# Kernel optimization log

Measured on AMD Instinct MI355X. Metric: run time of the kernel, lower is better.

## Reference

```python
import jax, jax.numpy as jnp
import numpy as np
import math

B, S, D, H, R = 4, 2048, 512, 8, 8  # R = k+1 relative slots per direction


def setup_inputs() -> dict:
    key = jax.random.key(0)
    ks = jax.random.split(key, 16)
    dk = D // H
    sc = 1.0 / math.sqrt(D)
    return {
        "query": jax.random.normal(ks[0], (B, S, D), jnp.float32),
        "key": jax.random.normal(ks[1], (B, S, D), jnp.float32),
        "value": jax.random.normal(ks[2], (B, S, D), jnp.float32),
        "start_nodes": jax.random.randint(ks[3], (B, H, R, S), 0, S, jnp.int64 if jax.config.jax_enable_x64 else jnp.int32),
        "end_nodes": jax.random.randint(ks[4], (B, H, R, S), 0, S, jnp.int64 if jax.config.jax_enable_x64 else jnp.int32),
        "rel_q": jax.random.normal(ks[5], (1, H, 2 * R, dk), jnp.float32),
        "rel_k": jax.random.normal(ks[6], (1, H, 2 * R, dk), jnp.float32),
        "rel_v": jax.random.normal(ks[7], (1, H, 2 * R, dk), jnp.float32),
        "Wq": jax.random.normal(ks[8], (D, D), jnp.float32) * sc,
        "bq": jnp.zeros((D,), jnp.float32),
        "Wk": jax.random.normal(ks[9], (D, D), jnp.float32) * sc,
        "bk": jnp.zeros((D,), jnp.float32),
        "Wv": jax.random.normal(ks[10], (D, D), jnp.float32) * sc,
        "bv": jnp.zeros((D,), jnp.float32),
        "Wo": jax.random.normal(ks[11], (D, D), jnp.float32) * sc,
        "bo": jnp.zeros((D,), jnp.float32),
    }


def reference(query, key, value, start_nodes, end_nodes, rel_q, rel_k, rel_v,
              Wq, bq, Wk, bk, Wv, bv, Wo, bo):
    Bs, Ss, Ds = query.shape
    Hs = start_nodes.shape[1]
    dk = Ds // Hs

    def proj(x, W, b):
        return (x @ W.T + b).reshape(Bs, Ss, Hs, dk).transpose(0, 2, 1, 3)  # [B,H,S,dk]

    q = proj(query, Wq, bq)
    k = proj(key, Wk, bk)
    v = proj(value, Wv, bv)

    start_mask = start_nodes == -1
    sn = jnp.where(start_mask, 0, start_nodes)  # -1 padding -> 0 (masked out below)
    qidx = jnp.concatenate([end_nodes, sn], axis=2)  # [B,H,2R,S]
    kidx = jnp.concatenate([sn, end_nodes], axis=2)

    bi = jnp.arange(Bs)[:, None, None, None]
    hi = jnp.arange(Hs)[None, :, None, None]
    q_ctx = q[bi, hi, qidx]  # [B,H,2R,S,dk]
    k_ctx = k[bi, hi, kidx]
    v_ctx = v[bi, hi, kidx]

    # c2c + c2p + p2c, scale_factor = 3 (rel_q and rel_k both provided)
    scores = ((q_ctx * k_ctx).sum(-1)
              + (q_ctx * rel_k[:, :, :, None, :]).sum(-1)
              + (rel_q[:, :, :, None, :] * k_ctx).sum(-1))
    scores = scores / (3.0 * jnp.sqrt(jnp.asarray(dk, scores.dtype)))

    # mask: padded edges masked in both halves; first S flat entries always masked
    mask = jnp.concatenate([start_mask, start_mask], axis=2).reshape(Bs, Hs, -1)
    mask = mask.at[:, :, :Ss].set(True)
    sflat = jnp.exp(jnp.where(mask, -1e9, scores.reshape(Bs, Hs, -1)))  # [B,H,2R*S]

    qf = qidx.reshape(Bs, Hs, -1)
    b2 = jnp.arange(Bs)[:, None, None]
    h2 = jnp.arange(Hs)[None, :, None]
    # scatter-add softmax denominator over destination nodes, then gather back
    denom = jnp.zeros((Bs, Hs, Ss), sflat.dtype).at[b2, h2, qf].add(sflat)
    denom = jnp.where(denom == 0, -1e9, denom)
    probs = (sflat / denom[b2, h2, qf]).reshape(Bs, Hs, -1, Ss, 1)  # [B,H,2R,S,1]

    attn_v = probs * (v_ctx + rel_v[:, :, :, None, :])  # [B,H,2R,S,dk]
    out = jnp.zeros((Bs, Hs, Ss, dk), attn_v.dtype).at[b2, h2, qf].add(
        attn_v.reshape(Bs, Hs, -1, dk))  # scatter-add aggregation over edges

    out = out.transpose(0, 2, 1, 3).reshape(Bs, Ss, Ds)
    return out @ Wo.T + bo
```

## Files before the change

### kernel.cpp

```cpp
#include <hip/hip_runtime.h>
#include <math.h>

#define B_ 4
#define S_ 2048
#define D_ 512
#define H_ 8
#define R_ 8
#define DK_ 64
#define EPB   (2*R_*S_)
#define ELLCAP 64

typedef __attribute__((ext_vector_type(8))) short bf16x8;
typedef __attribute__((ext_vector_type(8))) unsigned short ushort8_t;
typedef __attribute__((ext_vector_type(4))) float f32x4;

#define AS1q const __attribute__((address_space(1)))
#define AS3q __attribute__((address_space(3)))

__device__ inline unsigned short f2bf(float f) {
    unsigned u = __builtin_bit_cast(unsigned, f);
    u += 0x7fffu + ((u >> 16) & 1u);
    return (unsigned short)(u >> 16);
}

__global__ __launch_bounds__(256) void prep_w(
    const float* __restrict__ Wq, const float* __restrict__ Wk,
    const float* __restrict__ Wv, const float* __restrict__ Wo,
    unsigned short* __restrict__ wqb, unsigned short* __restrict__ wkb,
    unsigned short* __restrict__ wvb, unsigned short* __restrict__ wob)
{
    int bid = blockIdx.x;
    int z = bid >> 8;
    const float* x = (z == 0) ? Wq : (z == 1) ? Wk : (z == 2) ? Wv : Wo;
    unsigned short* y = (z == 0) ? wqb : (z == 1) ? wkb : (z == 2) ? wvb : wob;
    size_t i = ((size_t)(bid & 255) * 256 + threadIdx.x) * 4;
    float4 v = *(const float4*)&x[i];
    *(ushort4*)&y[i] = make_ushort4(f2bf(v.x), f2bf(v.y), f2bf(v.z), f2bf(v.w));
}

__global__ __launch_bounds__(256) void gemm_qkv(
    const float* __restrict__ A0, const float* __restrict__ A1,
    const float* __restrict__ A2,
    const unsigned short* __restrict__ W0, const unsigned short* __restrict__ W1,
    const unsigned short* __restrict__ W2,
    const float* __restrict__ bi0, const float* __restrict__ bi1, const float* __restrict__ bi2,
    float* __restrict__ C0, float* __restrict__ C1, float* __restrict__ C2)
{
    __shared__ unsigned short As[128 * 64];
    __shared__ unsigned short Bs[128 * 64];
    const int bi  = blockIdx.x;
    const int xcd = bi & 7;
    const int r   = bi >> 3;
    const int z   = r >> 5;
    const int rr  = r & 31;
    const int m0  = (xcd * 8 + (rr >> 2)) * 128;
    const int n0  = (rr & 3) * 128;

    const float* A          = (z == 0) ? A0 : (z == 1) ? A1 : A2;
    const unsigned short* W = (z == 0) ? W0 : (z == 1) ? W1 : W2;
    const float* bias       = (z == 0) ? bi0 : (z == 1) ? bi1 : bi2;
    float* C                = (z == 0) ? C0 : (z == 1) ? C1 : C2;

    const int t    = threadIdx.x;
    const int lane = t & 63;
    const int w    = t >> 6;
    const int wm   = w >> 1, wn = w & 1;
    const int lr    = lane >> 3;
    const int cglob = (lane & 7) ^ lr;

    f32x4 acc[4][4] = {};

    for (int kk = 0; kk < D_; kk += 64) {
        #pragma unroll
        for (int i = 0; i < 4; ++i) {
            int rowl = w * 32 + i * 8;
            const float* ga = A + (size_t)(m0 + rowl + lr) * D_ + kk + cglob * 8;
            float4 a0 = *(const float4*)ga;
            float4 a1 = *(const float4*)(ga + 4);
            ushort8_t c;
            c[0] = f2bf(a0.x); c[1] = f2bf(a0.y); c[2] = f2bf(a0.z); c[3] = f2bf(a0.w);
            c[4] = f2bf(a1.x); c[5] = f2bf(a1.y); c[6] = f2bf(a1.z); c[7] = f2bf(a1.w);
            *(ushort8_t*)&As[(rowl + lr) * 64 + (lane & 7) * 8] = c;
            const unsigned short* gb =
                W + (size_t)(n0 + rowl + lr) * D_ + kk + cglob * 8;
            __builtin_amdgcn_global_load_lds((AS1q unsigned*)gb,
                (AS3q unsigned*)(Bs + rowl * 64), 16, 0, 0);
        }
        __syncthreads();

        #pragma unroll
        for (int ks = 0; ks < 64; ks += 32) {
            const int c0 = ks >> 3;
            bf16x8 af[4], bfr[4];
            #pragma unroll
            for (int mi = 0; mi < 4; ++mi) {
                int row = wm * 64 + mi * 16 + (lane & 15);
                int cp  = (c0 + (lane >> 4)) ^ (lane & 7);
                af[mi] = *(const bf16x8*)&As[row * 64 + cp * 8];
            }
            #pragma unroll
            for (int nj = 0; nj < 4; ++nj) {
                int row = wn * 64 + nj * 16 + (lane & 15);
                int cp  = (c0 + (lane >> 4)) ^ (lane & 7);
                bfr[nj] = *(const bf16x8*)&Bs[row * 64 + cp * 8];
            }
            #pragma unroll
            for (int mi = 0; mi < 4; ++mi)
                #pragma unroll
                for (int nj = 0; nj < 4; ++nj)
                    acc[mi][nj] = __builtin_amdgcn_mfma_f32_16x16x32_bf16(af[mi], bfr[nj], acc[mi][nj], 0, 0, 0);
        }
        __syncthreads();
    }

    #pragma unroll
    for (int mi = 0; mi < 4; ++mi) {
        #pragma unroll
        for (int nj = 0; nj < 4; ++nj) {
            #pragma unroll
            for (int rg = 0; rg < 4; ++rg) {
                int m = m0 + wm * 64 + mi * 16 + (lane >> 4) * 4 + rg;
                int n = n0 + wn * 64 + nj * 16 + (lane & 15);
                float val = acc[mi][nj][rg] + bias[n];
                int b = m >> 11, s = m & (S_ - 1);
                int h = n >> 6,  d = n & 63;
                C[((((size_t)b * H_ + h) * S_ + s) << 6) + d] = val;
            }
        }
    }
}

__global__ __launch_bounds__(256) void gemm_out(
    const unsigned short* __restrict__ A, const unsigned short* __restrict__ W,
    const float* __restrict__ bias, float* __restrict__ Cf)
{
    __shared__ unsigned short As[128 * 64];
    __shared__ unsigned short Bs[64 * 64];
    const int bi  = blockIdx.x;
    const int xcd = bi & 7;
    const int r   = bi >> 3;
    const int m0  = (xcd * 8 + (r >> 3)) * 128;
    const int n0  = (r & 7) * 64;

    const int t    = threadIdx.x;
    const int lane = t & 63;
    const int w    = t >> 6;
    const int wm   = w >> 1, wn = w & 1;
    const int lr    = lane >> 3;
    const int cglob = (lane & 7) ^ lr;

    f32x4 acc[4][2] = {};

    for (int kk = 0; kk < D_; kk += 64) {
        #pragma unroll
        for (int i = 0; i < 4; ++i) {
            int rowl = w * 32 + i * 8;
            int m = m0 + rowl + lr;
            int b = m >> 11, s = m & (S_ - 1), h = kk >> 6;
            const unsigned short* ga =
                A + ((((size_t)b * H_ + h) * S_ + s) << 6) + cglob * 8;
            __builtin_amdgcn_global_load_lds((AS1q unsigned*)ga,
                (AS3q unsigned*)(As + rowl * 64), 16, 0, 0);
        }
        #pragma unroll
        for (int i = 0; i < 2; ++i) {
            int rowl = w * 16 + i * 8;
            const unsigned short* gb =
                W + (size_t)(n0 + rowl + lr) * D_ + kk + cglob * 8;
            __builtin_amdgcn_global_load_lds((AS1q unsigned*)gb,
                (AS3q unsigned*)(Bs + rowl * 64), 16, 0, 0);
        }
        __syncthreads();

        #pragma unroll
        for (int ks = 0; ks < 64; ks += 32) {
            const int c0 = ks >> 3;
            bf16x8 af[4], bfr[2];
            #pragma unroll
            for (int mi = 0; mi < 4; ++mi) {
                int row = wm * 64 + mi * 16 + (lane & 15);
                int cp  = (c0 + (lane >> 4)) ^ (lane & 7);
                af[mi] = *(const bf16x8*)&As[row * 64 + cp * 8];
            }
            #pragma unroll
            for (int nj = 0; nj < 2; ++nj) {
                int row = wn * 32 + nj * 16 + (lane & 15);
                int cp  = (c0 + (lane >> 4)) ^ (lane & 7);
                bfr[nj] = *(const bf16x8*)&Bs[row * 64 + cp * 8];
            }
            #pragma unroll
            for (int mi = 0; mi < 4; ++mi)
                #pragma unroll
                for (int nj = 0; nj < 2; ++nj)
                    acc[mi][nj] = __builtin_amdgcn_mfma_f32_16x16x32_bf16(af[mi], bfr[nj], acc[mi][nj], 0, 0, 0);
        }
        __syncthreads();
    }

    #pragma unroll
    for (int mi = 0; mi < 4; ++mi) {
        #pragma unroll
        for (int nj = 0; nj < 2; ++nj) {
            #pragma unroll
            for (int rg = 0; rg < 4; ++rg) {
                int m = m0 + wm * 64 + mi * 16 + (lane >> 4) * 4 + rg;
                int n = n0 + wn * 32 + nj * 16 + (lane & 15);
                Cf[(size_t)m * D_ + n] = acc[mi][nj][rg] + bias[n];
            }
        }
    }
}

__global__ __launch_bounds__(1024) void attn_fused(
    const float* __restrict__ q, const float* __restrict__ k_,
    const float* __restrict__ v_,
    const float* __restrict__ rel_q, const float* __restrict__ rel_k,
    const float* __restrict__ rel_v,
    const int* __restrict__ start_nodes, const int* __restrict__ end_nodes,
    unsigned short* __restrict__ attn)
{
    __shared__ unsigned short ell[128 * ELLCAP];
    __shared__ int cnt[128];
    const int bi  = blockIdx.x;
    const int xcd = bi & 7;
    const int loc = bi >> 3;
    const int bh  = xcd * 4 + (loc >> 4);
    const int dlo = (loc & 15) << 7;
    const int t   = threadIdx.x;

    if (t < 128) cnt[t] = 0;
    __syncthreads();

    const int base_idx = bh * (R_ * S_);
    for (int f = t; f < EPB; f += 1024) {
        int r2 = f >> 11;
        if (r2 == 0) continue;
        int s = f & (S_ - 1);
        int idx = base_idx + (r2 & 7) * S_ + s;
        int sn = start_nodes[idx];
        if (sn == -1) continue;
        int en = end_nodes[idx];
        int dst = (r2 < R_) ? en : sn;
        unsigned rel = (unsigned)(dst - dlo);
        if (rel < 128u) {
            int ki = (r2 < R_) ? sn : en;
            int pos = atomicAdd(&cnt[rel], 1);
            if (pos < ELLCAP)
                ell[(rel << 6) + pos] = (unsigned short)((r2 << 11) | ki);
        }
    }
    __syncthreads();

    const int w    = t >> 6;
    const int lane = t & 63;
    const int grp  = lane >> 3;
    const int sub  = lane & 7;
    const int h    = bh & 7;
    const size_t node_base = ((size_t)bh << 11);

    for (int dd = 0; dd < 8; ++dd) {
        int dl  = dd * 16 + w;
        int dst = dlo + dl;

        float qv[8];
        *(float4*)&qv[0] = *(const float4*)&q[((node_base + dst) << 6) + sub * 8];
        *(float4*)&qv[4] = *(const float4*)&q[((node_base + dst) << 6) + sub * 8 + 4];

        int n = cnt[dl];
        if (n > ELLCAP) n = ELLCAP;
        int d_all = (int)ell[(dl << 6) + lane];

        float den = 0.f;
        float o[8] = {};
        #pragma unroll 2
        for (int j = 0; j < n; j += 8) {
            int slot = j + grp;
            int d = __shfl(d_all, slot);
            bool valid = slot < n;
            int ki = d & (S_ - 1);
            int r2 = (d >> 11) & 15;
            size_t koff = ((node_base + ki) << 6) + sub * 8;
            int roff = (((h << 4) + r2) << 6) + sub * 8;
            float kv[8], rqv[8], rkv[8], vv[8], rvv[8];
            *(float4*)&kv[0]  = *(const float4*)&k_[koff];
            *(float4*)&kv[4]  = *(const float4*)&k_[koff + 4];
            *(float4*)&rqv[0] = *(const float4*)&rel_q[roff];
            *(float4*)&rqv[4] = *(const float4*)&rel_q[roff + 4];
            *(float4*)&rkv[0] = *(const float4*)&rel_k[roff];
            *(float4*)&rkv[4] = *(const float4*)&rel_k[roff + 4];
            float p = 0.f;
            #pragma unroll
            for (int i = 0; i < 8; ++i)
                p = fmaf(kv[i], qv[i] + rqv[i], fmaf(qv[i], rkv[i], p));
            p += __shfl_xor(p, 1);
            p += __shfl_xor(p, 2);
            p += __shfl_xor(p, 4);
            float sf = valid ? __expf(p * (1.0f / 24.0f)) : 0.f;
            *(float4*)&vv[0]  = *(const float4*)&v_[koff];
            *(float4*)&vv[4]  = *(const float4*)&v_[koff + 4];
            *(float4*)&rvv[0] = *(const float4*)&rel_v[roff];
            *(float4*)&rvv[4] = *(const float4*)&rel_v[roff + 4];
            den += sf;
            #pragma unroll
            for (int i = 0; i < 8; ++i)
                o[i] = fmaf(sf, vv[i] + rvv[i], o[i]);
        }
        den += __shfl_xor(den, 8); den += __shfl_xor(den, 16); den += __shfl_xor(den, 32);
        #pragma unroll
        for (int i = 0; i < 8; ++i) {
            o[i] += __shfl_xor(o[i], 8);
            o[i] += __shfl_xor(o[i], 16);
            o[i] += __shfl_xor(o[i], 32);
        }
        if (grp == 0) {
            float inv = (den > 0.f) ? 1.0f / den : 0.f;
            ushort8_t rs;
            #pragma unroll
            for (int i = 0; i < 8; ++i) rs[i] = f2bf(o[i] * inv);
            *(ushort8_t*)&attn[((node_base + dst) << 6) + sub * 8] = rs;
        }
    }
}

extern "C" void kernel_launch(void* const* d_in, const int* in_sizes, int n_in,
                              void* d_out, int out_size, void* d_ws, size_t ws_size,
                              hipStream_t stream) {
    const float* query = (const float*)d_in[0];
    const float* key   = (const float*)d_in[1];
    const float* value = (const float*)d_in[2];
    const int* start_nodes = (const int*)d_in[3];
    const int* end_nodes   = (const int*)d_in[4];
    const float* rel_q = (const float*)d_in[5];
    const float* rel_k = (const float*)d_in[6];
    const float* rel_v = (const float*)d_in[7];
    const float* Wq = (const float*)d_in[8];
    const float* bq = (const float*)d_in[9];
    const float* Wk = (const float*)d_in[10];
    const float* bk = (const float*)d_in[11];
    const float* Wv = (const float*)d_in[12];
    const float* bv = (const float*)d_in[13];
    const float* Wo = (const float*)d_in[14];
    const float* bo = (const float*)d_in[15];
    float* out = (float*)d_out;

    const size_t NQ = (size_t)B_ * H_ * S_ * DK_;
    const size_t NW = (size_t)D_ * D_;
    float* qf = (float*)d_ws;
    float* kf = qf + NQ;
    float* vf = kf + NQ;
    unsigned short* attn = (unsigned short*)(vf + NQ);
    unsigned short* wqb  = attn + NQ;
    unsigned short* wkb  = wqb + NW;
    unsigned short* wvb  = wkb + NW;
    unsigned short* wob  = wvb + NW;

    prep_w<<<1024, 256, 0, stream>>>(Wq, Wk, Wv, Wo, wqb, wkb, wvb, wob);

    gemm_qkv<<<768, 256, 0, stream>>>(query, key, value, wqb, wkb, wvb,
                                      bq, bk, bv, qf, kf, vf);

    attn_fused<<<512, 1024, 0, stream>>>(qf, kf, vf, rel_q, rel_k, rel_v,
                                         start_nodes, end_nodes, attn);

    gemm_out<<<512, 256, 0, stream>>>(attn, wob, bo, out);
}
```

Baseline: 237.0 us.

## Store Q/K/V and rel tables in bf16 and pre-pack weights into MFMA fragment layout

```diff
diff --git a/kernel.cpp b/kernel.cpp
--- a/kernel.cpp
+++ b/kernel.cpp
@@ -22,32 +22,71 @@
     u += 0x7fffu + ((u >> 16) & 1u);
     return (unsigned short)(u >> 16);
 }
-
-__global__ __launch_bounds__(256) void prep_w(
+__device__ inline float bf2f(unsigned short u) {
+    return __builtin_bit_cast(float, ((unsigned)u) << 16);
+}
+
+__global__ __launch_bounds__(256) void prep(
+    const float* __restrict__ query, const float* __restrict__ key,
+    const float* __restrict__ value,
     const float* __restrict__ Wq, const float* __restrict__ Wk,
     const float* __restrict__ Wv, const float* __restrict__ Wo,
-    unsigned short* __restrict__ wqb, unsigned short* __restrict__ wkb,
-    unsigned short* __restrict__ wvb, unsigned short* __restrict__ wob)
+    const float* __restrict__ rel_q, const float* __restrict__ rel_k,
+    const float* __restrict__ rel_v,
+    unsigned short* __restrict__ qc, unsigned short* __restrict__ kc_,
+    unsigned short* __restrict__ vc,
+    unsigned short* __restrict__ wqp, unsigned short* __restrict__ wkp,
+    unsigned short* __restrict__ wvp, unsigned short* __restrict__ wop,
+    unsigned short* __restrict__ rqb, unsigned short* __restrict__ rkb,
+    unsigned short* __restrict__ rvb)
 {
     int bid = blockIdx.x;
-    int z = bid >> 8;
-    const float* x = (z == 0) ? Wq : (z == 1) ? Wk : (z == 2) ? Wv : Wo;
-    unsigned short* y = (z == 0) ? wqb : (z == 1) ? wkb : (z == 2) ? wvb : wob;
-    size_t i = ((size_t)(bid & 255) * 256 + threadIdx.x) * 4;
-    float4 v = *(const float4*)&x[i];
-    *(ushort4*)&y[i] = make_ushort4(f2bf(v.x), f2bf(v.y), f2bf(v.z), f2bf(v.w));
+    int t = threadIdx.x;
+    if (bid < 12288) {
+        int z = bid >> 12;
+        const float* x = (z == 0) ? query : (z == 1) ? key : value;
+        unsigned short* y = (z == 0) ? qc : (z == 1) ? kc_ : vc;
+        size_t i = ((size_t)(bid & 4095) * 256 + t) * 4;
+        float4 v = *(const float4*)&x[i];
+        *(ushort4*)&y[i] = make_ushort4(f2bf(v.x), f2bf(v.y), f2bf(v.z), f2bf(v.w));
+    } else if (bid < 12800) {
+        int r = bid - 12288;
+        int z = r >> 7;
+        const float* x = (z == 0) ? Wq : (z == 1) ? Wk : (z == 2) ? Wv : Wo;
+        unsigned short* y = (z == 0) ? wqp : (z == 1) ? wkp : (z == 2) ? wvp : wop;
+        int fi = (r & 127) * 256 + t;
+        int ng   = fi >> 10;
+        int kc   = (fi >> 6) & 15;
+        int lane = fi & 63;
+        const float* src = x + (size_t)(ng * 16 + (lane & 15)) * D_
+                             + kc * 32 + (lane >> 4) * 8;
+        float4 a0 = *(const float4*)src;
+        float4 a1 = *(const float4*)(src + 4);
+        ushort8_t c;
+        c[0] = f2bf(a0.x); c[1] = f2bf(a0.y); c[2] = f2bf(a0.z); c[3] = f2bf(a0.w);
+        c[4] = f2bf(a1.x); c[5] = f2bf(a1.y); c[6] = f2bf(a1.z); c[7] = f2bf(a1.w);
+        *(ushort8_t*)&y[(size_t)fi * 8] = c;
+    } else {
+        int rr = bid - 12800;
+        int z = rr >> 3;
+        const float* x = (z == 0) ? rel_q : (z == 1) ? rel_k : rel_v;
+        unsigned short* y = (z == 0) ? rqb : (z == 1) ? rkb : rvb;
+        size_t i = ((size_t)(rr & 7) * 256 + t) * 4;
+        float4 v = *(const float4*)&x[i];
+        *(ushort4*)&y[i] = make_ushort4(f2bf(v.x), f2bf(v.y), f2bf(v.z), f2bf(v.w));
+    }
 }
 
 __global__ __launch_bounds__(256) void gemm_qkv(
-    const float* __restrict__ A0, const float* __restrict__ A1,
-    const float* __restrict__ A2,
+    const unsigned short* __restrict__ A0, const unsigned short* __restrict__ A1,
+    const unsigned short* __restrict__ A2,
     const unsigned short* __restrict__ W0, const unsigned short* __restrict__ W1,
     const unsigned short* __restrict__ W2,
     const float* __restrict__ bi0, const float* __restrict__ bi1, const float* __restrict__ bi2,
-    float* __restrict__ C0, float* __restrict__ C1, float* __restrict__ C2)
+    unsigned short* __restrict__ C0, unsigned short* __restrict__ C1,
+    unsigned short* __restrict__ C2)
 {
     __shared__ unsigned short As[128 * 64];
-    __shared__ unsigned short Bs[128 * 64];
     const int bi  = blockIdx.x;
     const int xcd = bi & 7;
     const int r   = bi >> 3;
@@ -56,10 +95,10 @@
     const int m0  = (xcd * 8 + (rr >> 2)) * 128;
     const int n0  = (rr & 3) * 128;
 
-    const float* A          = (z == 0) ? A0 : (z == 1) ? A1 : A2;
+    const unsigned short* A = (z == 0) ? A0 : (z == 1) ? A1 : A2;
     const unsigned short* W = (z == 0) ? W0 : (z == 1) ? W1 : W2;
     const float* bias       = (z == 0) ? bi0 : (z == 1) ? bi1 : bi2;
-    float* C                = (z == 0) ? C0 : (z == 1) ? C1 : C2;
+    unsigned short* C       = (z == 0) ? C0 : (z == 1) ? C1 : C2;
 
     const int t    = threadIdx.x;
     const int lane = t & 63;
@@ -74,23 +113,17 @@
         #pragma unroll
         for (int i = 0; i < 4; ++i) {
             int rowl = w * 32 + i * 8;
-            const float* ga = A + (size_t)(m0 + rowl + lr) * D_ + kk + cglob * 8;
-            float4 a0 = *(const float4*)ga;
-            float4 a1 = *(const float4*)(ga + 4);
-            ushort8_t c;
-            c[0] = f2bf(a0.x); c[1] = f2bf(a0.y); c[2] = f2bf(a0.z); c[3] = f2bf(a0.w);
-            c[4] = f2bf(a1.x); c[5] = f2bf(a1.y); c[6] = f2bf(a1.z); c[7] = f2bf(a1.w);
-            *(ushort8_t*)&As[(rowl + lr) * 64 + (lane & 7) * 8] = c;
-            const unsigned short* gb =
-                W + (size_t)(n0 + rowl + lr) * D_ + kk + cglob * 8;
-            __builtin_amdgcn_global_load_lds((AS1q unsigned*)gb,
-                (AS3q unsigned*)(Bs + rowl * 64), 16, 0, 0);
+            const unsigned short* ga =
+                A + (size_t)(m0 + rowl + lr) * D_ + kk + cglob * 8;
+            __builtin_amdgcn_global_load_lds((AS1q unsigned*)ga,
+                (AS3q unsigned*)(As + rowl * 64), 16, 0, 0);
         }
         __syncthreads();
 
         #pragma unroll
         for (int ks = 0; ks < 64; ks += 32) {
             const int c0 = ks >> 3;
+            const int kc = (kk + ks) >> 5;
             bf16x8 af[4], bfr[4];
             #pragma unroll
             for (int mi = 0; mi < 4; ++mi) {
@@ -100,9 +133,8 @@
             }
             #pragma unroll
             for (int nj = 0; nj < 4; ++nj) {
-                int row = wn * 64 + nj * 16 + (lane & 15);
-                int cp  = (c0 + (lane >> 4)) ^ (lane & 7);
-                bfr[nj] = *(const bf16x8*)&Bs[row * 64 + cp * 8];
+                int ng = (n0 >> 4) + wn * 4 + nj;
+                bfr[nj] = *(const bf16x8*)&W[(size_t)((ng * 16 + kc) << 6) * 8 + lane * 8];
             }
             #pragma unroll
             for (int mi = 0; mi < 4; ++mi)
@@ -124,7 +156,7 @@
                 float val = acc[mi][nj][rg] + bias[n];
                 int b = m >> 11, s = m & (S_ - 1);
                 int h = n >> 6,  d = n & 63;
-                C[((((size_t)b * H_ + h) * S_ + s) << 6) + d] = val;
+                C[((((size_t)b * H_ + h) * S_ + s) << 6) + d] = f2bf(val);
             }
         }
     }
@@ -135,7 +167,6 @@
     const float* __restrict__ bias, float* __restrict__ Cf)
 {
     __shared__ unsigned short As[128 * 64];
-    __shared__ unsigned short Bs[64 * 64];
     const int bi  = blockIdx.x;
     const int xcd = bi & 7;
     const int r   = bi >> 3;
@@ -162,19 +193,12 @@
             __builtin_amdgcn_global_load_lds((AS1q unsigned*)ga,
                 (AS3q unsigned*)(As + rowl * 64), 16, 0, 0);
         }
-        #pragma unroll
-        for (int i = 0; i < 2; ++i) {
-            int rowl = w * 16 + i * 8;
-            const unsigned short* gb =
-                W + (size_t)(n0 + rowl + lr) * D_ + kk + cglob * 8;
-            __builtin_amdgcn_global_load_lds((AS1q unsigned*)gb,
-                (AS3q unsigned*)(Bs + rowl * 64), 16, 0, 0);
-        }
         __syncthreads();
 
         #pragma unroll
         for (int ks = 0; ks < 64; ks += 32) {
             const int c0 = ks >> 3;
+            const int kc = (kk + ks) >> 5;
             bf16x8 af[4], bfr[2];
             #pragma unroll
             for (int mi = 0; mi < 4; ++mi) {
@@ -184,9 +208,8 @@
             }
             #pragma unroll
             for (int nj = 0; nj < 2; ++nj) {
-                int row = wn * 32 + nj * 16 + (lane & 15);
-                int cp  = (c0 + (lane >> 4)) ^ (lane & 7);
-                bfr[nj] = *(const bf16x8*)&Bs[row * 64 + cp * 8];
+                int ng = (n0 >> 4) + wn * 2 + nj;
+                bfr[nj] = *(const bf16x8*)&W[(size_t)((ng * 16 + kc) << 6) * 8 + lane * 8];
             }
             #pragma unroll
             for (int mi = 0; mi < 4; ++mi)
@@ -212,10 +235,10 @@
 }
 
 __global__ __launch_bounds__(1024) void attn_fused(
-    const float* __restrict__ q, const float* __restrict__ k_,
-    const float* __restrict__ v_,
-    const float* __restrict__ rel_q, const float* __restrict__ rel_k,
-    const float* __restrict__ rel_v,
+    const unsigned short* __restrict__ q, const unsigned short* __restrict__ k_,
+    const unsigned short* __restrict__ v_,
+    const unsigned short* __restrict__ rel_q, const unsigned short* __restrict__ rel_k,
+    const unsigned short* __restrict__ rel_v,
     const int* __restrict__ start_nodes, const int* __restrict__ end_nodes,
     unsigned short* __restrict__ attn)
 {
@@ -262,9 +285,10 @@
         int dl  = dd * 16 + w;
         int dst = dlo + dl;
 
+        ushort8_t q8 = *(const ushort8_t*)&q[((node_base + dst) << 6) + sub * 8];
         float qv[8];
-        *(float4*)&qv[0] = *(const float4*)&q[((node_base + dst) << 6) + sub * 8];
-        *(float4*)&qv[4] = *(const float4*)&q[((node_base + dst) << 6) + sub * 8 + 4];
+        #pragma unroll
+        for (int i = 0; i < 8; ++i) qv[i] = bf2f(q8[i]);
 
         int n = cnt[dl];
         if (n > ELLCAP) n = ELLCAP;
@@ -279,31 +303,24 @@
             bool valid = slot < n;
             int ki = d & (S_ - 1);
             int r2 = (d >> 11) & 15;
-            size_t koff = ((node_base + ki) << 6) + sub * 8;
-            int roff = (((h << 4) + r2) << 6) + sub * 8;
-            float kv[8], rqv[8], rkv[8], vv[8], rvv[8];
-            *(float4*)&kv[0]  = *(const float4*)&k_[koff];
-            *(float4*)&kv[4]  = *(const float4*)&k_[koff + 4];
-            *(float4*)&rqv[0] = *(const float4*)&rel_q[roff];
-            *(float4*)&rqv[4] = *(const float4*)&rel_q[roff + 4];
-            *(float4*)&rkv[0] = *(const float4*)&rel_k[roff];
-            *(float4*)&rkv[4] = *(const float4*)&rel_k[roff + 4];
+            ushort8_t k8  = *(const ushort8_t*)&k_  [((node_base + ki) << 6) + sub * 8];
+            ushort8_t rk8 = *(const ushort8_t*)&rel_k[(((h << 4) + r2) << 6) + sub * 8];
+            ushort8_t rq8 = *(const ushort8_t*)&rel_q[(((h << 4) + r2) << 6) + sub * 8];
             float p = 0.f;
             #pragma unroll
             for (int i = 0; i < 8; ++i)
-                p = fmaf(kv[i], qv[i] + rqv[i], fmaf(qv[i], rkv[i], p));
+                p = fmaf(bf2f(k8[i]), qv[i] + bf2f(rq8[i]),
+                         fmaf(qv[i], bf2f(rk8[i]), p));
             p += __shfl_xor(p, 1);
             p += __shfl_xor(p, 2);
             p += __shfl_xor(p, 4);
             float sf = valid ? __expf(p * (1.0f / 24.0f)) : 0.f;
-            *(float4*)&vv[0]  = *(const float4*)&v_[koff];
-            *(float4*)&vv[4]  = *(const float4*)&v_[koff + 4];
-            *(float4*)&rvv[0] = *(const float4*)&rel_v[roff];
-            *(float4*)&rvv[4] = *(const float4*)&rel_v[roff + 4];
+            ushort8_t v8  = *(const ushort8_t*)&v_  [((node_base + ki) << 6) + sub * 8];
+            ushort8_t rv8 = *(const ushort8_t*)&rel_v[(((h << 4) + r2) << 6) + sub * 8];
             den += sf;
             #pragma unroll
             for (int i = 0; i < 8; ++i)
-                o[i] = fmaf(sf, vv[i] + rvv[i], o[i]);
+                o[i] = fmaf(sf, bf2f(v8[i]) + bf2f(rv8[i]), o[i]);
         }
         den += __shfl_xor(den, 8); den += __shfl_xor(den, 16); den += __shfl_xor(den, 32);
         #pragma unroll
@@ -345,22 +362,33 @@
 
     const size_t NQ = (size_t)B_ * H_ * S_ * DK_;
     const size_t NW = (size_t)D_ * D_;
-    float* qf = (float*)d_ws;
-    float* kf = qf + NQ;
-    float* vf = kf + NQ;
-    unsigned short* attn = (unsigned short*)(vf + NQ);
-    unsigned short* wqb  = attn + NQ;
-    unsigned short* wkb  = wqb + NW;
-    unsigned short* wvb  = wkb + NW;
-    unsigned short* wob  = wvb + NW;
-
-    prep_w<<<1024, 256, 0, stream>>>(Wq, Wk, Wv, Wo, wqb, wkb, wvb, wob);
-
-    gemm_qkv<<<768, 256, 0, stream>>>(query, key, value, wqb, wkb, wvb,
-                                      bq, bk, bv, qf, kf, vf);
-
-    attn_fused<<<512, 1024, 0, stream>>>(qf, kf, vf, rel_q, rel_k, rel_v,
+    const size_t NR = (size_t)H_ * 2 * R_ * DK_;
+    unsigned short* p = (unsigned short*)d_ws;
+    unsigned short* qc = p;            p += NQ;
+    unsigned short* kc = p;            p += NQ;
+    unsigned short* vc = p;            p += NQ;
+    unsigned short* q  = p;            p += NQ;
+    unsigned short* k  = p;            p += NQ;
+    unsigned short* v  = p;            p += NQ;
+    unsigned short* attn = p;          p += NQ;
+    unsigned short* wqp = p;           p += NW;
+    unsigned short* wkp = p;           p += NW;
+    unsigned short* wvp = p;           p += NW;
+    unsigned short* wop = p;           p += NW;
+    unsigned short* rqb = p;           p += NR;
+    unsigned short* rkb = p;           p += NR;
+    unsigned short* rvb = p;           p += NR;
+
+    prep<<<12824, 256, 0, stream>>>(query, key, value, Wq, Wk, Wv, Wo,
+                                    rel_q, rel_k, rel_v,
+                                    qc, kc, vc, wqp, wkp, wvp, wop,
+                                    rqb, rkb, rvb);
+
+    gemm_qkv<<<768, 256, 0, stream>>>(qc, kc, vc, wqp, wkp, wvp,
+                                      bq, bk, bv, q, k, v);
+
+    attn_fused<<<512, 1024, 0, stream>>>(q, k, v, rqb, rkb, rvb,
                                          start_nodes, end_nodes, attn);
 
-    gemm_out<<<512, 256, 0, stream>>>(attn, wob, bo, out);
-}
+    gemm_out<<<512, 256, 0, stream>>>(attn, wop, bo, out);
+}
```

After: 223.5 us. 1.06x faster.
